# Performance work log

Hardware: AMD Instinct MI355X
Metric: run time of the kernel (lower is better)

The kernel has to match this reference:

```python
import jax, jax.numpy as jnp
import numpy as np

T, H, E, K, I, S = 512, 1024, 32, 4, 512, 2048  # tokens, hidden, experts, top_k, moe_inter, shared_inter


def setup_inputs() -> dict:
    key = jax.random.key(0)
    ks = jax.random.split(key, 8)
    sc = 0.02
    return {
        "hidden_states": jax.random.normal(ks[0], (T, H), jnp.float32),
        "Wg": jax.random.normal(ks[1], (H, E + 1), jnp.float32) * sc,          # router gate + shared gate (merged)
        "W_gate": jax.random.normal(ks[2], (E, H, I), jnp.float32) * sc,        # per-expert gate proj
        "W_up": jax.random.normal(ks[3], (E, H, I), jnp.float32) * sc,          # per-expert up proj
        "W_down": jax.random.normal(ks[4], (E, I, H), jnp.float32) * sc,        # per-expert down proj
        "Ws_gate": jax.random.normal(ks[5], (H, S), jnp.float32) * sc,          # shared expert gate proj
        "Ws_up": jax.random.normal(ks[6], (H, S), jnp.float32) * sc,            # shared expert up proj
        "Ws_down": jax.random.normal(ks[7], (S, H), jnp.float32) * sc,          # shared expert down proj
    }


def reference(hidden_states, Wg, W_gate, W_up, W_down, Ws_gate, Ws_up, Ws_down):
    x = hidden_states  # [T, H]
    logits = x @ Wg                       # [T, E+1]
    router_logits = logits[:, :E]         # [T, E]
    shared_gate_logits = logits[:, E:]    # [T, 1]

    # top-k softmax routing with renormalization (renormalize=True)
    probs = jax.nn.softmax(router_logits, axis=-1)          # [T, E]
    topk_w, topk_idx = jax.lax.top_k(probs, K)               # [T, K]
    topk_w = topk_w / jnp.sum(topk_w, axis=-1, keepdims=True)
    combine = jnp.zeros((T, E), x.dtype).at[jnp.arange(T)[:, None], topk_idx].add(topk_w)  # [T, E]

    # routed experts: dense reference over all experts, combined by routing weights
    g = jnp.einsum("th,ehi->eti", x, W_gate)                 # [E, T, I]
    u = jnp.einsum("th,ehi->eti", x, W_up)                   # [E, T, I]
    h = jax.nn.silu(g) * u                                    # SiluAndMul
    y = jnp.einsum("eti,eih->eth", h, W_down)                # [E, T, H]
    routed = jnp.einsum("te,eth->th", combine, y)            # [T, H]

    # shared expert MLP + sigmoid shared-gate
    sh = (jax.nn.silu(x @ Ws_gate) * (x @ Ws_up)) @ Ws_down  # [T, H]
    shared = jax.nn.sigmoid(shared_gate_logits) * sh

    return shared + routed
```

## Files before the change

kernel.cpp:

```cpp
#include <hip/hip_runtime.h>
#include <hip/hip_bf16.h>

#define TT 512
#define HH 1024
#define EE 32
#define KK 4
#define II 512
#define SS 2048

using f32x4 = __attribute__((ext_vector_type(4))) float;
using s16x8 = __attribute__((ext_vector_type(8))) short;

__device__ __forceinline__ unsigned short f2bf(float f){
  unsigned int u = __builtin_bit_cast(unsigned int, f);
  u += 0x7fffu + ((u >> 16) & 1u);
  return (unsigned short)(u >> 16);
}

__device__ __forceinline__ uint4 pack8(const unsigned short* u){
  uint4 v;
  v.x = (unsigned)u[0] | ((unsigned)u[1] << 16);
  v.y = (unsigned)u[2] | ((unsigned)u[3] << 16);
  v.z = (unsigned)u[4] | ((unsigned)u[5] << 16);
  v.w = (unsigned)u[6] | ((unsigned)u[7] << 16);
  return v;
}

__global__ __launch_bounds__(64) void k_router(
    const float* __restrict__ x, const float* __restrict__ Wg,
    unsigned short* __restrict__ xb, int* __restrict__ topk_idx,
    float* __restrict__ topk_w, float* __restrict__ sig_gate){
  int t = blockIdx.x; int l = threadIdx.x;
  const float* xr = x + (size_t)t * HH;
  #pragma unroll
  for(int i=0;i<HH/64;i++){
    int h = l + 64*i;
    xb[(size_t)t*HH + h] = f2bf(xr[h]);
  }
  float acc0=0.f, acc1=0.f, acc2=0.f, acc3=0.f;
  if(l < EE+1){
    const float* wcol = Wg + l;
    for(int h=0; h<HH; h+=4){
      acc0 += xr[h]   * wcol[(size_t)h*(EE+1)];
      acc1 += xr[h+1] * wcol[(size_t)(h+1)*(EE+1)];
      acc2 += xr[h+2] * wcol[(size_t)(h+2)*(EE+1)];
      acc3 += xr[h+3] * wcol[(size_t)(h+3)*(EE+1)];
    }
  }
  __shared__ float lg[EE+1];
  if(l < EE+1) lg[l] = (acc0+acc1)+(acc2+acc3);
  __syncthreads();
  if(l == 0){
    float v[EE];
    #pragma unroll
    for(int i=0;i<EE;i++) v[i]=lg[i];
    int idx[KK]; float val[KK];
    #pragma unroll
    for(int k=0;k<KK;k++){
      float m=-1e30f; int mi=0;
      for(int i=0;i<EE;i++){ if(v[i]>m){ m=v[i]; mi=i; } }
      idx[k]=mi; val[k]=m; v[mi]=-1e30f;
    }
    float mx = val[0], s=0.f; float w[KK];
    #pragma unroll
    for(int k=0;k<KK;k++){ w[k]=__expf(val[k]-mx); s+=w[k]; }
    float inv = 1.f/s;
    #pragma unroll
    for(int k=0;k<KK;k++){ topk_idx[t*KK+k]=idx[k]; topk_w[t*KK+k]=w[k]*inv; }
    sig_gate[t] = 1.f/(1.f+__expf(-lg[EE]));
  }
}

__global__ __launch_bounds__(64) void k_build(
    const int* __restrict__ topk_idx, const float* __restrict__ topk_w,
    int* __restrict__ token_list, float* __restrict__ weight_list,
    int* __restrict__ counts){
  int e = blockIdx.x; int l = threadIdx.x;
  int cnt = 0;
  for(int c=0;c<TT;c+=64){
    int t = c + l;
    int kk = -1;
    #pragma unroll
    for(int k=0;k<KK;k++) if(topk_idx[t*KK+k]==e) kk=k;
    unsigned long long b = __ballot(kk>=0);
    int pre = __popcll(b & ((1ull<<l)-1ull));
    if(kk>=0){
      token_list[e*TT + cnt + pre] = t;
      weight_list[e*TT + cnt + pre] = topk_w[t*KK+kk];
    }
    cnt += __popcll(b);
  }
  if(l==0) counts[e]=cnt;
}

__device__ __forceinline__ void wrb(unsigned short B[64][40], const float* f,
                                    int n, int kh){
  unsigned short u[8];
  #pragma unroll
  for(int i=0;i<8;i++) u[i] = f2bf(f[i]);
  *reinterpret_cast<uint4*>(&B[n][kh*8]) = pack8(u);
}

__device__ __forceinline__ void gemm_dual(
    const unsigned short* Ap, bool va,
    const float* Gp, const float* Up, int ldb, int NK,
    f32x4* ag, f32x4* au,
    unsigned short As[2][64][40], unsigned short Bg[2][64][40],
    unsigned short Bu[2][64][40], int tid){
  int w = tid>>6, l = tid&63;
  int n = tid&63, kh = tid>>6, ar = tid>>2, as_ = tid&3;
  uint4 av = make_uint4(0,0,0,0);
  float gv[8], uv[8];
  if(va) av = *reinterpret_cast<const uint4*>(Ap);
  #pragma unroll
  for(int i=0;i<8;i++){ gv[i]=Gp[(size_t)i*ldb]; uv[i]=Up[(size_t)i*ldb]; }
  *reinterpret_cast<uint4*>(&As[0][ar][as_*8]) = av;
  wrb(Bg[0], gv, n, kh); wrb(Bu[0], uv, n, kh);
  __syncthreads();
  for(int ks=0; ks<NK; ks++){
    int cur = ks & 1;
    bool more = (ks+1 < NK);
    if(more){
      av = make_uint4(0,0,0,0);
      if(va) av = *reinterpret_cast<const uint4*>(Ap + (size_t)(ks+1)*32);
      const float* g2 = Gp + (size_t)(ks+1)*32*ldb;
      const float* u2 = Up + (size_t)(ks+1)*32*ldb;
      #pragma unroll
      for(int i=0;i<8;i++){ gv[i]=g2[(size_t)i*ldb]; uv[i]=u2[(size_t)i*ldb]; }
    }
    int kt = l>>4, mm = l&15;
    s16x8 af = *reinterpret_cast<const s16x8*>(&As[cur][w*16+mm][kt*8]);
    #pragma unroll
    for(int c=0;c<4;c++){
      s16x8 b0 = *reinterpret_cast<const s16x8*>(&Bg[cur][c*16+mm][kt*8]);
      s16x8 b1 = *reinterpret_cast<const s16x8*>(&Bu[cur][c*16+mm][kt*8]);
      ag[c] = __builtin_amdgcn_mfma_f32_16x16x32_bf16(af, b0, ag[c], 0,0,0);
      au[c] = __builtin_amdgcn_mfma_f32_16x16x32_bf16(af, b1, au[c], 0,0,0);
    }
    if(more){
      int nx = cur^1;
      *reinterpret_cast<uint4*>(&As[nx][ar][as_*8]) = av;
      wrb(Bg[nx], gv, n, kh); wrb(Bu[nx], uv, n, kh);
    }
    __syncthreads();
  }
}

__device__ __forceinline__ void gemm_single(
    const unsigned short* Ap, bool va,
    const float* Bp, int ldb, int NK, f32x4* acc,
    unsigned short As[2][64][40], unsigned short Bs[2][64][40], int tid){
  int w = tid>>6, l = tid&63;
  int n = tid&63, kh = tid>>6, ar = tid>>2, as_ = tid&3;
  uint4 av = make_uint4(0,0,0,0);
  float bv[8];
  if(va) av = *reinterpret_cast<const uint4*>(Ap);
  #pragma unroll
  for(int i=0;i<8;i++) bv[i] = Bp[(size_t)i*ldb];
  *reinterpret_cast<uint4*>(&As[0][ar][as_*8]) = av;
  wrb(Bs[0], bv, n, kh);
  __syncthreads();
  for(int ks=0; ks<NK; ks++){
    int cur = ks & 1;
    bool more = (ks+1 < NK);
    if(more){
      av = make_uint4(0,0,0,0);
      if(va) av = *reinterpret_cast<const uint4*>(Ap + (size_t)(ks+1)*32);
      const float* b2 = Bp + (size_t)(ks+1)*32*ldb;
      #pragma unroll
      for(int i=0;i<8;i++) bv[i] = b2[(size_t)i*ldb];
    }
    int kt = l>>4, mm = l&15;
    s16x8 af = *reinterpret_cast<const s16x8*>(&As[cur][w*16+mm][kt*8]);
    #pragma unroll
    for(int c=0;c<4;c++){
      s16x8 b0 = *reinterpret_cast<const s16x8*>(&Bs[cur][c*16+mm][kt*8]);
      acc[c] = __builtin_amdgcn_mfma_f32_16x16x32_bf16(af, b0, acc[c], 0,0,0);
    }
    if(more){
      int nx = cur^1;
      *reinterpret_cast<uint4*>(&As[nx][ar][as_*8]) = av;
      wrb(Bs[nx], bv, n, kh);
    }
    __syncthreads();
  }
}

__global__ __launch_bounds__(256) void k_gateup_all(
    const unsigned short* __restrict__ xb,
    const float* __restrict__ Wsg, const float* __restrict__ Wsu,
    unsigned short* __restrict__ Hs,
    const float* __restrict__ Wgate, const float* __restrict__ Wup,
    const int* __restrict__ token_list, const int* __restrict__ counts,
    unsigned short* __restrict__ hbuf){
  __shared__ unsigned short As[2][64][40];
  __shared__ unsigned short Bg[2][64][40];
  __shared__ unsigned short Bu[2][64][40];
  int tid = threadIdx.x, w = tid>>6, l = tid&63;
  int n = tid&63, kh = tid>>6, ar = tid>>2, as_ = tid&3;
  int bid = blockIdx.x;
  f32x4 zero = {0.f,0.f,0.f,0.f};
  const int NSH = (SS/64)*(TT/64);

  if(bid < NSH){
    int n0 = (bid & (SS/64 - 1)) * 64;
    int r0 = (bid / (SS/64)) * 64;
    f32x4 ag[4]={zero,zero,zero,zero}, au[4]={zero,zero,zero,zero};
    const unsigned short* Ap = xb + (size_t)(r0+ar)*HH + as_*8;
    const float* Gp = Wsg + (size_t)(kh*8)*SS + n0 + n;
    const float* Up = Wsu + (size_t)(kh*8)*SS + n0 + n;
    gemm_dual(Ap, true, Gp, Up, SS, HH/32, ag, au, As, Bg, Bu, tid);
    int mm = l&15, rb = r0 + w*16 + (l>>4)*4;
    #pragma unroll
    for(int c=0;c<4;c++){
      #pragma unroll
      for(int j=0;j<4;j++){
        float g = ag[c][j], u = au[c][j];
        Hs[(size_t)(rb+j)*SS + n0 + c*16 + mm] = f2bf(g*u/(1.f+__expf(-g)));
      }
    }
  } else {
    int b = bid - NSH;
    int e = b >> 3;
    int i0 = (b & 7) * 64;
    int cnt = counts[e]; if(cnt == 0) return;
    int off = 0;
    for(int i=0;i<e;i++) off += counts[i];
    const float* Bg0 = Wgate + (size_t)e*HH*II;
    const float* Bu0 = Wup   + (size_t)e*HH*II;
    for(int rt=0; rt*64<cnt; rt++){
      int nv = cnt - rt*64; if(nv > 64) nv = 64;
      const int* rows = token_list + e*TT + rt*64;
      int arow = (ar < nv) ? rows[ar] : 0;
      bool va = ar < nv;
      f32x4 ag[4]={zero,zero,zero,zero}, au[4]={zero,zero,zero,zero};
      const unsigned short* Ap = xb + (size_t)arow*HH + as_*8;
      const float* Gp = Bg0 + (size_t)(kh*8)*II + i0 + n;
      const float* Up = Bu0 + (size_t)(kh*8)*II + i0 + n;
      gemm_dual(Ap, va, Gp, Up, II, HH/32, ag, au, As, Bg, Bu, tid);
      int mm = l&15, rr0 = w*16 + (l>>4)*4;
      #pragma unroll
      for(int c=0;c<4;c++){
        #pragma unroll
        for(int j=0;j<4;j++){
          int rr = rr0 + j;
          if(rr < nv){
            float g = ag[c][j], u = au[c][j];
            hbuf[(size_t)(off+rt*64+rr)*II + i0 + c*16 + mm] =
                f2bf(g*u/(1.f+__expf(-g)));
          }
        }
      }
    }
  }
}

__global__ __launch_bounds__(256) void k_down_all(
    const unsigned short* __restrict__ Hsrc, const float* __restrict__ Wsd,
    const float* __restrict__ sig_gate,
    const unsigned short* __restrict__ hbuf, const float* __restrict__ Wdown,
    const int* __restrict__ token_list, const float* __restrict__ weight_list,
    const int* __restrict__ counts, float* __restrict__ out){
  __shared__ unsigned short As[2][64][40];
  __shared__ unsigned short Bs[2][64][40];
  int tid = threadIdx.x, w = tid>>6, l = tid&63;
  int n = tid&63, kh = tid>>6, ar = tid>>2, as_ = tid&3;
  int bid = blockIdx.x;
  f32x4 zero = {0.f,0.f,0.f,0.f};
  const int NSH = (HH/64)*(TT/64);

  if(bid < NSH){
    int n0 = (bid & (HH/64 - 1)) * 64;
    int r0 = (bid / (HH/64)) * 64;
    f32x4 acc[4]={zero,zero,zero,zero};
    const unsigned short* Ap = Hsrc + (size_t)(r0+ar)*SS + as_*8;
    const float* Bp = Wsd + (size_t)(kh*8)*HH + n0 + n;
    gemm_single(Ap, true, Bp, HH, SS/32, acc, As, Bs, tid);
    int mm = l&15, rb = r0 + w*16 + (l>>4)*4;
    #pragma unroll
    for(int c=0;c<4;c++){
      #pragma unroll
      for(int j=0;j<4;j++){
        atomicAdd(&out[(size_t)(rb+j)*HH + n0 + c*16 + mm],
                  sig_gate[rb+j]*acc[c][j]);
      }
    }
  } else {
    int b = bid - NSH;
    int e = b >> 4;
    int n0 = (b & 15) * 64;
    int cnt = counts[e]; if(cnt == 0) return;
    int off = 0;
    for(int i=0;i<e;i++) off += counts[i];
    const float* B0 = Wdown + (size_t)e*II*HH;
    for(int rt=0; rt*64<cnt; rt++){
      int nv = cnt - rt*64; if(nv > 64) nv = 64;
      bool va = ar < nv;
      f32x4 acc[4]={zero,zero,zero,zero};
      const unsigned short* Ap = hbuf + (size_t)(off+rt*64+ar)*II + as_*8;
      const float* Bp = B0 + (size_t)(kh*8)*HH + n0 + n;
      gemm_single(Ap, va, Bp, HH, II/32, acc, As, Bs, tid);
      int mm = l&15, rr0 = w*16 + (l>>4)*4;
      #pragma unroll
      for(int c=0;c<4;c++){
        #pragma unroll
        for(int j=0;j<4;j++){
          int rr = rr0 + j;
          if(rr < nv){
            int t = token_list[e*TT + rt*64 + rr];
            float wt = weight_list[e*TT + rt*64 + rr];
            atomicAdd(&out[(size_t)t*HH + n0 + c*16 + mm], wt*acc[c][j]);
          }
        }
      }
    }
  }
}

extern "C" void kernel_launch(void* const* d_in, const int* in_sizes, int n_in,
                              void* d_out, int out_size, void* d_ws, size_t ws_size,
                              hipStream_t stream) {
  const float* x     = (const float*)d_in[0];
  const float* Wg    = (const float*)d_in[1];
  const float* Wgate = (const float*)d_in[2];
  const float* Wup   = (const float*)d_in[3];
  const float* Wdown = (const float*)d_in[4];
  const float* Wsg   = (const float*)d_in[5];
  const float* Wsu   = (const float*)d_in[6];
  const float* Wsd   = (const float*)d_in[7];
  float* out = (float*)d_out;

  char* ws = (char*)d_ws;
  unsigned short* xb   = (unsigned short*)ws; ws += (size_t)TT*HH*2;
  unsigned short* Hs   = (unsigned short*)ws; ws += (size_t)TT*SS*2;
  unsigned short* hbuf = (unsigned short*)ws; ws += (size_t)(TT*KK+64)*II*2;
  int*   token_list  = (int*)ws;   ws += (size_t)EE*TT*4;
  float* weight_list = (float*)ws; ws += (size_t)EE*TT*4;
  int*   topk_idx    = (int*)ws;   ws += (size_t)TT*KK*4;
  float* topk_wq     = (float*)ws; ws += (size_t)TT*KK*4;
  int*   counts      = (int*)ws;   ws += 128;
  float* sig_gate    = (float*)ws; ws += (size_t)TT*4;

  hipMemsetAsync(d_out, 0, (size_t)TT*HH*4, stream);
  k_router<<<TT, 64, 0, stream>>>(x, Wg, xb, topk_idx, topk_wq, sig_gate);
  k_build<<<EE, 64, 0, stream>>>(topk_idx, topk_wq, token_list, weight_list, counts);
  k_gateup_all<<<(SS/64)*(TT/64) + EE*(II/64), 256, 0, stream>>>(
      xb, Wsg, Wsu, Hs, Wgate, Wup, token_list, counts, hbuf);
  k_down_all<<<(HH/64)*(TT/64) + EE*(HH/64), 256, 0, stream>>>(
      Hs, Wsd, sig_gate, hbuf, Wdown, token_list, weight_list, counts, out);
}
```

Before: 146.5 us.

## Use 128-row tiles for shared expert GEMMs to reuse weight tiles

```diff
diff --git a/kernel.cpp b/kernel.cpp
--- a/kernel.cpp
+++ b/kernel.cpp
@@ -17,12 +17,12 @@
   return (unsigned short)(u >> 16);
 }
 
-__device__ __forceinline__ uint4 pack8(const unsigned short* u){
+__device__ __forceinline__ uint4 cvt8(const float* f){
   uint4 v;
-  v.x = (unsigned)u[0] | ((unsigned)u[1] << 16);
-  v.y = (unsigned)u[2] | ((unsigned)u[3] << 16);
-  v.z = (unsigned)u[4] | ((unsigned)u[5] << 16);
-  v.w = (unsigned)u[6] | ((unsigned)u[7] << 16);
+  v.x = (unsigned)f2bf(f[0]) | ((unsigned)f2bf(f[1])<<16);
+  v.y = (unsigned)f2bf(f[2]) | ((unsigned)f2bf(f[3])<<16);
+  v.z = (unsigned)f2bf(f[4]) | ((unsigned)f2bf(f[5])<<16);
+  v.w = (unsigned)f2bf(f[6]) | ((unsigned)f2bf(f[7])<<16);
   return v;
 }
 
@@ -93,94 +93,70 @@
   if(l==0) counts[e]=cnt;
 }
 
-__device__ __forceinline__ void wrb(unsigned short B[64][40], const float* f,
-                                    int n, int kh){
-  unsigned short u[8];
+template<int RG, bool DUAL>
+__device__ __forceinline__ void gemm64(
+    const unsigned short* A0, const unsigned short* A1, bool va,
+    const float* Gp, const float* Up, int ldb, int NK,
+    f32x4 (*ag)[4], f32x4 (*au)[4],
+    unsigned short* As, unsigned short* Bg, unsigned short* Bu, int tid){
+  const int MR = RG*64;
+  const int w = tid>>6, l = tid&63;
+  const int n = tid&63, kh = tid>>6, ar = tid>>2, as_ = tid&3;
+  const int kt = l>>4, mm = l&15;
+  uint4 av0 = make_uint4(0,0,0,0), av1 = make_uint4(0,0,0,0);
+  float gv[8], uv[8];
+  if(va) av0 = *reinterpret_cast<const uint4*>(A0);
+  if(RG==2) av1 = *reinterpret_cast<const uint4*>(A1);
   #pragma unroll
-  for(int i=0;i<8;i++) u[i] = f2bf(f[i]);
-  *reinterpret_cast<uint4*>(&B[n][kh*8]) = pack8(u);
-}
-
-__device__ __forceinline__ void gemm_dual(
-    const unsigned short* Ap, bool va,
-    const float* Gp, const float* Up, int ldb, int NK,
-    f32x4* ag, f32x4* au,
-    unsigned short As[2][64][40], unsigned short Bg[2][64][40],
-    unsigned short Bu[2][64][40], int tid){
-  int w = tid>>6, l = tid&63;
-  int n = tid&63, kh = tid>>6, ar = tid>>2, as_ = tid&3;
-  uint4 av = make_uint4(0,0,0,0);
-  float gv[8], uv[8];
-  if(va) av = *reinterpret_cast<const uint4*>(Ap);
-  #pragma unroll
-  for(int i=0;i<8;i++){ gv[i]=Gp[(size_t)i*ldb]; uv[i]=Up[(size_t)i*ldb]; }
-  *reinterpret_cast<uint4*>(&As[0][ar][as_*8]) = av;
-  wrb(Bg[0], gv, n, kh); wrb(Bu[0], uv, n, kh);
+  for(int i=0;i<8;i++) gv[i] = Gp[(size_t)i*ldb];
+  if(DUAL){
+    #pragma unroll
+    for(int i=0;i<8;i++) uv[i] = Up[(size_t)i*ldb];
+  }
+  *reinterpret_cast<uint4*>(As + (size_t)ar*40 + as_*8) = av0;
+  if(RG==2) *reinterpret_cast<uint4*>(As + (size_t)(64+ar)*40 + as_*8) = av1;
+  *reinterpret_cast<uint4*>(Bg + (size_t)n*40 + kh*8) = cvt8(gv);
+  if(DUAL) *reinterpret_cast<uint4*>(Bu + (size_t)n*40 + kh*8) = cvt8(uv);
   __syncthreads();
   for(int ks=0; ks<NK; ks++){
-    int cur = ks & 1;
-    bool more = (ks+1 < NK);
+    const int cur = ks & 1;
+    const bool more = (ks+1 < NK);
     if(more){
-      av = make_uint4(0,0,0,0);
-      if(va) av = *reinterpret_cast<const uint4*>(Ap + (size_t)(ks+1)*32);
-      const float* g2 = Gp + (size_t)(ks+1)*32*ldb;
-      const float* u2 = Up + (size_t)(ks+1)*32*ldb;
-      #pragma unroll
-      for(int i=0;i<8;i++){ gv[i]=g2[(size_t)i*ldb]; uv[i]=u2[(size_t)i*ldb]; }
-    }
-    int kt = l>>4, mm = l&15;
-    s16x8 af = *reinterpret_cast<const s16x8*>(&As[cur][w*16+mm][kt*8]);
+      av0 = make_uint4(0,0,0,0);
+      if(va) av0 = *reinterpret_cast<const uint4*>(A0 + (size_t)(ks+1)*32);
+      if(RG==2) av1 = *reinterpret_cast<const uint4*>(A1 + (size_t)(ks+1)*32);
+      const float* g = Gp + (size_t)(ks+1)*32*ldb;
+      #pragma unroll
+      for(int i=0;i<8;i++) gv[i] = g[(size_t)i*ldb];
+      if(DUAL){
+        const float* u = Up + (size_t)(ks+1)*32*ldb;
+        #pragma unroll
+        for(int i=0;i<8;i++) uv[i] = u[(size_t)i*ldb];
+      }
+    }
+    s16x8 bg_[4], bu_[4];
     #pragma unroll
     for(int c=0;c<4;c++){
-      s16x8 b0 = *reinterpret_cast<const s16x8*>(&Bg[cur][c*16+mm][kt*8]);
-      s16x8 b1 = *reinterpret_cast<const s16x8*>(&Bu[cur][c*16+mm][kt*8]);
-      ag[c] = __builtin_amdgcn_mfma_f32_16x16x32_bf16(af, b0, ag[c], 0,0,0);
-      au[c] = __builtin_amdgcn_mfma_f32_16x16x32_bf16(af, b1, au[c], 0,0,0);
+      bg_[c] = *reinterpret_cast<const s16x8*>(Bg + ((size_t)cur*64 + c*16 + mm)*40 + kt*8);
+      if(DUAL)
+        bu_[c] = *reinterpret_cast<const s16x8*>(Bu + ((size_t)cur*64 + c*16 + mm)*40 + kt*8);
+    }
+    #pragma unroll
+    for(int rg=0; rg<RG; rg++){
+      s16x8 af = *reinterpret_cast<const s16x8*>(As + ((size_t)cur*MR + rg*64 + w*16 + mm)*40 + kt*8);
+      #pragma unroll
+      for(int c=0;c<4;c++){
+        ag[rg][c] = __builtin_amdgcn_mfma_f32_16x16x32_bf16(af, bg_[c], ag[rg][c], 0,0,0);
+        if(DUAL)
+          au[rg][c] = __builtin_amdgcn_mfma_f32_16x16x32_bf16(af, bu_[c], au[rg][c], 0,0,0);
+      }
     }
     if(more){
-      int nx = cur^1;
-      *reinterpret_cast<uint4*>(&As[nx][ar][as_*8]) = av;
-      wrb(Bg[nx], gv, n, kh); wrb(Bu[nx], uv, n, kh);
-    }
-    __syncthreads();
-  }
-}
-
-__device__ __forceinline__ void gemm_single(
-    const unsigned short* Ap, bool va,
-    const float* Bp, int ldb, int NK, f32x4* acc,
-    unsigned short As[2][64][40], unsigned short Bs[2][64][40], int tid){
-  int w = tid>>6, l = tid&63;
-  int n = tid&63, kh = tid>>6, ar = tid>>2, as_ = tid&3;
-  uint4 av = make_uint4(0,0,0,0);
-  float bv[8];
-  if(va) av = *reinterpret_cast<const uint4*>(Ap);
-  #pragma unroll
-  for(int i=0;i<8;i++) bv[i] = Bp[(size_t)i*ldb];
-  *reinterpret_cast<uint4*>(&As[0][ar][as_*8]) = av;
-  wrb(Bs[0], bv, n, kh);
-  __syncthreads();
-  for(int ks=0; ks<NK; ks++){
-    int cur = ks & 1;
-    bool more = (ks+1 < NK);
-    if(more){
-      av = make_uint4(0,0,0,0);
-      if(va) av = *reinterpret_cast<const uint4*>(Ap + (size_t)(ks+1)*32);
-      const float* b2 = Bp + (size_t)(ks+1)*32*ldb;
-      #pragma unroll
-      for(int i=0;i<8;i++) bv[i] = b2[(size_t)i*ldb];
-    }
-    int kt = l>>4, mm = l&15;
-    s16x8 af = *reinterpret_cast<const s16x8*>(&As[cur][w*16+mm][kt*8]);
-    #pragma unroll
-    for(int c=0;c<4;c++){
-      s16x8 b0 = *reinterpret_cast<const s16x8*>(&Bs[cur][c*16+mm][kt*8]);
-      acc[c] = __builtin_amdgcn_mfma_f32_16x16x32_bf16(af, b0, acc[c], 0,0,0);
-    }
-    if(more){
-      int nx = cur^1;
-      *reinterpret_cast<uint4*>(&As[nx][ar][as_*8]) = av;
-      wrb(Bs[nx], bv, n, kh);
+      const int nx = cur^1;
+      *reinterpret_cast<uint4*>(As + ((size_t)nx*MR + ar)*40 + as_*8) = av0;
+      if(RG==2) *reinterpret_cast<uint4*>(As + ((size_t)nx*MR + 64 + ar)*40 + as_*8) = av1;
+      *reinterpret_cast<uint4*>(Bg + ((size_t)nx*64 + n)*40 + kh*8) = cvt8(gv);
+      if(DUAL) *reinterpret_cast<uint4*>(Bu + ((size_t)nx*64 + n)*40 + kh*8) = cvt8(uv);
     }
     __syncthreads();
   }
@@ -193,30 +169,39 @@
     const float* __restrict__ Wgate, const float* __restrict__ Wup,
     const int* __restrict__ token_list, const int* __restrict__ counts,
     unsigned short* __restrict__ hbuf){
-  __shared__ unsigned short As[2][64][40];
-  __shared__ unsigned short Bg[2][64][40];
-  __shared__ unsigned short Bu[2][64][40];
+  __shared__ unsigned short As[2*128*40];
+  __shared__ unsigned short Bg[2*64*40];
+  __shared__ unsigned short Bu[2*64*40];
   int tid = threadIdx.x, w = tid>>6, l = tid&63;
-  int n = tid&63, kh = tid>>6, ar = tid>>2, as_ = tid&3;
+  int ar = tid>>2, as_ = tid&3, n = tid&63, kh = tid>>6;
   int bid = blockIdx.x;
   f32x4 zero = {0.f,0.f,0.f,0.f};
-  const int NSH = (SS/64)*(TT/64);
+  const int NSH = (TT/128)*(SS/64);
 
   if(bid < NSH){
-    int n0 = (bid & (SS/64 - 1)) * 64;
-    int r0 = (bid / (SS/64)) * 64;
-    f32x4 ag[4]={zero,zero,zero,zero}, au[4]={zero,zero,zero,zero};
-    const unsigned short* Ap = xb + (size_t)(r0+ar)*HH + as_*8;
+    int n0 = (bid & 31) * 64;
+    int r0 = (bid >> 5) * 128;
+    f32x4 ag[2][4], au[2][4];
+    #pragma unroll
+    for(int rg=0;rg<2;rg++)
+      #pragma unroll
+      for(int c=0;c<4;c++){ ag[rg][c]=zero; au[rg][c]=zero; }
+    const unsigned short* A0 = xb + (size_t)(r0+ar)*HH + as_*8;
+    const unsigned short* A1 = A0 + (size_t)64*HH;
     const float* Gp = Wsg + (size_t)(kh*8)*SS + n0 + n;
     const float* Up = Wsu + (size_t)(kh*8)*SS + n0 + n;
-    gemm_dual(Ap, true, Gp, Up, SS, HH/32, ag, au, As, Bg, Bu, tid);
-    int mm = l&15, rb = r0 + w*16 + (l>>4)*4;
-    #pragma unroll
-    for(int c=0;c<4;c++){
-      #pragma unroll
-      for(int j=0;j<4;j++){
-        float g = ag[c][j], u = au[c][j];
-        Hs[(size_t)(rb+j)*SS + n0 + c*16 + mm] = f2bf(g*u/(1.f+__expf(-g)));
+    gemm64<2,true>(A0, A1, true, Gp, Up, SS, HH/32, ag, au, As, Bg, Bu, tid);
+    int mm = l&15;
+    #pragma unroll
+    for(int rg=0;rg<2;rg++){
+      int rb = r0 + rg*64 + w*16 + (l>>4)*4;
+      #pragma unroll
+      for(int c=0;c<4;c++){
+        #pragma unroll
+        for(int j=0;j<4;j++){
+          float g = ag[rg][c][j], u = au[rg][c][j];
+          Hs[(size_t)(rb+j)*SS + n0 + c*16 + mm] = f2bf(g*u/(1.f+__expf(-g)));
+        }
       }
     }
   } else {
@@ -233,11 +218,13 @@
       const int* rows = token_list + e*TT + rt*64;
       int arow = (ar < nv) ? rows[ar] : 0;
       bool va = ar < nv;
-      f32x4 ag[4]={zero,zero,zero,zero}, au[4]={zero,zero,zero,zero};
-      const unsigned short* Ap = xb + (size_t)arow*HH + as_*8;
+      f32x4 ag[1][4], au[1][4];
+      #pragma unroll
+      for(int c=0;c<4;c++){ ag[0][c]=zero; au[0][c]=zero; }
+      const unsigned short* A0 = xb + (size_t)arow*HH + as_*8;
       const float* Gp = Bg0 + (size_t)(kh*8)*II + i0 + n;
       const float* Up = Bu0 + (size_t)(kh*8)*II + i0 + n;
-      gemm_dual(Ap, va, Gp, Up, II, HH/32, ag, au, As, Bg, Bu, tid);
+      gemm64<1,true>(A0, A0, va, Gp, Up, II, HH/32, ag, au, As, Bg, Bu, tid);
       int mm = l&15, rr0 = w*16 + (l>>4)*4;
       #pragma unroll
       for(int c=0;c<4;c++){
@@ -245,7 +232,7 @@
         for(int j=0;j<4;j++){
           int rr = rr0 + j;
           if(rr < nv){
-            float g = ag[c][j], u = au[c][j];
+            float g = ag[0][c][j], u = au[0][c][j];
             hbuf[(size_t)(off+rt*64+rr)*II + i0 + c*16 + mm] =
                 f2bf(g*u/(1.f+__expf(-g)));
           }
@@ -261,28 +248,37 @@
     const unsigned short* __restrict__ hbuf, const float* __restrict__ Wdown,
     const int* __restrict__ token_list, const float* __restrict__ weight_list,
     const int* __restrict__ counts, float* __restrict__ out){
-  __shared__ unsigned short As[2][64][40];
-  __shared__ unsigned short Bs[2][64][40];
+  __shared__ unsigned short As[2*128*40];
+  __shared__ unsigned short Bs[2*64*40];
   int tid = threadIdx.x, w = tid>>6, l = tid&63;
-  int n = tid&63, kh = tid>>6, ar = tid>>2, as_ = tid&3;
+  int ar = tid>>2, as_ = tid&3, n = tid&63, kh = tid>>6;
   int bid = blockIdx.x;
   f32x4 zero = {0.f,0.f,0.f,0.f};
-  const int NSH = (HH/64)*(TT/64);
+  const int NSH = (TT/128)*(HH/64);
 
   if(bid < NSH){
-    int n0 = (bid & (HH/64 - 1)) * 64;
-    int r0 = (bid / (HH/64)) * 64;
-    f32x4 acc[4]={zero,zero,zero,zero};
-    const unsigned short* Ap = Hsrc + (size_t)(r0+ar)*SS + as_*8;
+    int n0 = (bid & 15) * 64;
+    int r0 = (bid >> 4) * 128;
+    f32x4 acc[2][4];
+    #pragma unroll
+    for(int rg=0;rg<2;rg++)
+      #pragma unroll
+      for(int c=0;c<4;c++) acc[rg][c]=zero;
+    const unsigned short* A0 = Hsrc + (size_t)(r0+ar)*SS + as_*8;
+    const unsigned short* A1 = A0 + (size_t)64*SS;
     const float* Bp = Wsd + (size_t)(kh*8)*HH + n0 + n;
-    gemm_single(Ap, true, Bp, HH, SS/32, acc, As, Bs, tid);
-    int mm = l&15, rb = r0 + w*16 + (l>>4)*4;
-    #pragma unroll
-    for(int c=0;c<4;c++){
-      #pragma unroll
-      for(int j=0;j<4;j++){
-        atomicAdd(&out[(size_t)(rb+j)*HH + n0 + c*16 + mm],
-                  sig_gate[rb+j]*acc[c][j]);
+    gemm64<2,false>(A0, A1, true, Bp, Bp, HH, SS/32, acc, acc, As, Bs, Bs, tid);
+    int mm = l&15;
+    #pragma unroll
+    for(int rg=0;rg<2;rg++){
+      int rb = r0 + rg*64 + w*16 + (l>>4)*4;
+      #pragma unroll
+      for(int c=0;c<4;c++){
+        #pragma unroll
+        for(int j=0;j<4;j++){
+          atomicAdd(&out[(size_t)(rb+j)*HH + n0 + c*16 + mm],
+                    sig_gate[rb+j]*acc[rg][c][j]);
+        }
       }
     }
   } else {
@@ -296,10 +292,12 @@
     for(int rt=0; rt*64<cnt; rt++){
       int nv = cnt - rt*64; if(nv > 64) nv = 64;
       bool va = ar < nv;
-      f32x4 acc[4]={zero,zero,zero,zero};
-      const unsigned short* Ap = hbuf + (size_t)(off+rt*64+ar)*II + as_*8;
+      f32x4 acc[1][4];
+      #pragma unroll
+      for(int c=0;c<4;c++) acc[0][c]=zero;
+      const unsigned short* A0 = hbuf + (size_t)(off+rt*64+ar)*II + as_*8;
       const float* Bp = B0 + (size_t)(kh*8)*HH + n0 + n;
-      gemm_single(Ap, va, Bp, HH, II/32, acc, As, Bs, tid);
+      gemm64<1,false>(A0, A0, va, Bp, Bp, HH, II/32, acc, acc, As, Bs, Bs, tid);
       int mm = l&15, rr0 = w*16 + (l>>4)*4;
       #pragma unroll
       for(int c=0;c<4;c++){
@@ -309,7 +307,7 @@
           if(rr < nv){
             int t = token_list[e*TT + rt*64 + rr];
             float wt = weight_list[e*TT + rt*64 + rr];
-            atomicAdd(&out[(size_t)t*HH + n0 + c*16 + mm], wt*acc[c][j]);
+            atomicAdd(&out[(size_t)t*HH + n0 + c*16 + mm], wt*acc[0][c][j]);
           }
         }
       }
@@ -344,8 +342,8 @@
   hipMemsetAsync(d_out, 0, (size_t)TT*HH*4, stream);
   k_router<<<TT, 64, 0, stream>>>(x, Wg, xb, topk_idx, topk_wq, sig_gate);
   k_build<<<EE, 64, 0, stream>>>(topk_idx, topk_wq, token_list, weight_list, counts);
-  k_gateup_all<<<(SS/64)*(TT/64) + EE*(II/64), 256, 0, stream>>>(
+  k_gateup_all<<<(TT/128)*(SS/64) + EE*(II/64), 256, 0, stream>>>(
       xb, Wsg, Wsu, Hs, Wgate, Wup, token_list, counts, hbuf);
-  k_down_all<<<(HH/64)*(TT/64) + EE*(HH/64), 256, 0, stream>>>(
+  k_down_all<<<(TT/128)*(HH/64) + EE*(HH/64), 256, 0, stream>>>(
       Hs, Wsd, sig_gate, hbuf, Wdown, token_list, weight_list, counts, out);
 }
```

After: 151.4 us. 3.4% more time.
